# Kernel tuning notes

Hardware: AMD Instinct MI355X
Metric: run time of the kernel (lower is better)

The kernel has to match this reference:

```python
import jax, jax.numpy as jnp
import numpy as np

N = 50000      # nodes
E = 800000     # edges (avg degree 16)
F_IN = 128     # num_features
H = 128        # hidden_channels
C = 64         # num_classes
K = 3          # TAGConv hops (PyG default)


def setup_inputs() -> dict:
    key = jax.random.key(0)
    k0, k1, k2, k3 = jax.random.split(key, 4)
    x = jax.random.normal(k0, (N, F_IN), dtype=jnp.float32)
    edge_index = jax.random.randint(k1, (2, E), 0, N, dtype=jnp.int32)
    W1 = jax.random.normal(k2, (K + 1, F_IN, H), dtype=jnp.float32) / np.sqrt(F_IN).astype(np.float32)
    b1 = jnp.zeros((H,), dtype=jnp.float32)
    W2 = jax.random.normal(k3, (K + 1, H, C), dtype=jnp.float32) / np.sqrt(H).astype(np.float32)
    b2 = jnp.zeros((C,), dtype=jnp.float32)
    return {"x": x, "edge_index": edge_index, "W1": W1, "b1": b1, "W2": W2, "b2": b2}


def _gcn_norm(row, col):
    # PyG gcn_norm with add_self_loops=False (TAGConv default):
    # deg over target nodes (col), norm = d^-1/2[row] * d^-1/2[col]
    deg = jax.ops.segment_sum(jnp.ones((E,), dtype=jnp.float32), col, num_segments=N)
    dinv = jnp.where(deg > 0, jax.lax.rsqrt(jnp.maximum(deg, 1.0)) * jnp.where(deg > 0, 1.0, 0.0), 0.0)
    dinv = jnp.where(deg > 0, deg ** -0.5, 0.0)
    return dinv[row] * dinv[col]


def _tag_conv(h, row, col, norm, W, b):
    # out = sum_{k=0..K} A_hat^k h @ W[k] + b, A_hat = D^-1/2 A D^-1/2
    out = h @ W[0]
    for k in range(1, K + 1):
        h = jax.ops.segment_sum(norm[:, None] * h[row], col, num_segments=N)  # [N, d]
        out = out + h @ W[k]
    return out + b


def reference(x, edge_index, W1, b1, W2, b2):
    row, col = edge_index[0], edge_index[1]
    norm = _gcn_norm(row, col)  # [E]
    h = jax.nn.relu(_tag_conv(x, row, col, norm, W1, b1))
    # F.dropout with training=False is the identity (inference reference)
    out = _tag_conv(h, row, col, norm, W2, b2)
    return jax.nn.log_softmax(out, axis=1)
```

## Files before the change

### kernel.cpp

```cpp
#include <hip/hip_runtime.h>
#include <stdint.h>

#define NN 50000
#define EE 800000
#define NROWS 50048
#define CB 196
#define CAP 5120
#define ACH 4096

typedef unsigned int u32;
typedef unsigned short u16;
using f32x4 = __attribute__((ext_vector_type(4))) float;
using short8 = __attribute__((ext_vector_type(8))) short;

__device__ __forceinline__ float bflo(u32 u) { return __uint_as_float(u << 16); }
__device__ __forceinline__ float bfhi(u32 u) { return __uint_as_float(u & 0xFFFF0000u); }
__device__ __forceinline__ float bf1(u16 v) { return __uint_as_float(((u32)v) << 16); }
__device__ __forceinline__ u32 f2bf(float f) {
    u32 u = __float_as_uint(f);
    return (u + 0x7FFFu + ((u >> 16) & 1u)) >> 16;
}
__device__ __forceinline__ u32 pack2(float lo, float hi) {
    return f2bf(lo) | (f2bf(hi) << 16);
}

__device__ __forceinline__ int excl_scan256(int v, int tid) {
    __shared__ int ws_[4];
    int lane = tid & 63, w = tid >> 6;
    int x = v;
    #pragma unroll
    for (int off = 1; off < 64; off <<= 1) {
        int y = __shfl_up(x, off, 64);
        if (lane >= off) x += y;
    }
    if (lane == 63) ws_[w] = x;
    __syncthreads();
    int add = 0;
    if (w > 0) add += ws_[0];
    if (w > 1) add += ws_[1];
    if (w > 2) add += ws_[2];
    return add + x - v;
}


__global__ void detect_kernel(const u32* __restrict__ xw, int* __restrict__ flag) {
    int tid = threadIdx.x;
    int cnt = 0;
    for (int i = tid; i < 8192; i += 256) {
        u32 u = xw[i];
        int e0 = (u >> 7) & 0xFF, e1 = (u >> 23) & 0xFF;
        cnt += (e0 >= 0xC3) + (e1 >= 0xC3);
    }
    #pragma unroll
    for (int off = 32; off; off >>= 1) cnt += __shfl_xor(cnt, off, 64);
    __shared__ int wsum[4];
    if ((tid & 63) == 0) wsum[tid >> 6] = cnt;
    __syncthreads();
    if (tid == 0) flag[0] = (wsum[0] + wsum[1] + wsum[2] + wsum[3] > 100) ? 1 : 0;
}


__global__ __launch_bounds__(256) void phaseA_kernel(const int* __restrict__ ei,
                                                     int* __restrict__ ccnt,
                                                     u32* __restrict__ cpad) {
    __shared__ int hist[256], lstart[256], lofs[256], gbase[256];
    __shared__ u32 srt[ACH];
    int tid = threadIdx.x;
    int e0 = blockIdx.x * ACH;
    int nv = EE - e0; if (nv > ACH) nv = ACH;
    hist[tid] = 0;
    __syncthreads();
    u32 pk[16];
    int bn[16];
    #pragma unroll
    for (int i = 0; i < 16; i++) {
        int e = e0 + tid + i * 256;
        bn[i] = -1;
        if (e < EE) {
            int r = ei[e], c = ei[EE + e];
            bn[i] = c >> 8;
            pk[i] = (u32)r | ((u32)(c & 255) << 16) | ((u32)bn[i] << 24);
            atomicAdd(&hist[bn[i]], 1);
        }
    }
    __syncthreads();
    int v = hist[tid];
    int excl = excl_scan256(v, tid);
    lstart[tid] = excl;
    lofs[tid] = excl;
    gbase[tid] = atomicAdd(&ccnt[tid], v);
    __syncthreads();
    #pragma unroll
    for (int i = 0; i < 16; i++)
        if (bn[i] >= 0) {
            int lp = atomicAdd(&lofs[bn[i]], 1);
            srt[lp] = pk[i];
        }
    __syncthreads();
    for (int j = tid; j < nv; j += 256) {
        u32 pv = srt[j];
        int b = pv >> 24;
        cpad[(size_t)b * CAP + gbase[b] + (j - lstart[b])] = pv;
    }
}

__global__ void cscan_kernel(const int* __restrict__ ccnt, int* __restrict__ cbase,
                             int* __restrict__ rowptr, float* __restrict__ dinv) {
    int tid = threadIdx.x;
    int v = ccnt[tid];
    int excl = excl_scan256(v, tid);
    cbase[tid] = excl;
    if (tid == 0) {
        rowptr[NN] = EE;
        rowptr[NN + 1] = EE;
        dinv[NN] = 0.f;
    }
}


__global__ __launch_bounds__(256) void phaseB_kernel(const u32* __restrict__ cpad,
                                                     const int* __restrict__ ccnt,
                                                     const int* __restrict__ cbase,
                                                     u16* __restrict__ esrc,
                                                     int* __restrict__ rowptr,
                                                     float* __restrict__ dinv,
                                                     float* __restrict__ rinv) {
    __shared__ int hist[256], lstart[256], lofs[256];
    __shared__ u16 srt[CAP];
    int tid = threadIdx.x, cb = blockIdx.x;
    int cnt = ccnt[cb], base = cbase[cb];
    hist[tid] = 0;
    __syncthreads();
    for (int j = tid; j < cnt; j += 256)
        atomicAdd(&hist[(cpad[(size_t)cb * CAP + j] >> 16) & 255], 1);
    __syncthreads();
    int v = hist[tid];
    int excl = excl_scan256(v, tid);
    lstart[tid] = excl;
    lofs[tid] = excl;
    int g = cb * 256 + tid;
    if (g < NN) {
        rowptr[g] = base + excl;
        dinv[g] = v > 0 ? rsqrtf((float)v) : 0.f;
        rinv[g] = v > 0 ? sqrtf((float)v) : 0.f;
    }
    __syncthreads();
    for (int j = tid; j < cnt; j += 256) {
        u32 pv = cpad[(size_t)cb * CAP + j];
        int lp = atomicAdd(&lofs[(pv >> 16) & 255], 1);
        srt[lp] = (u16)(pv & 0xFFFF);
    }
    __syncthreads();
    for (int j = tid; j < cnt; j += 256) esrc[base + j] = srt[j];
}

__global__ void wprep_kernel(const void* __restrict__ w, u16* __restrict__ wt,
                             int fout, int nk, int mode, int total,
                             const int* __restrict__ flag) {
    int idx = blockIdx.x * 256 + threadIdx.x;
    if (idx >= total) return;
    u16 v = flag[0] ? (u16)f2bf(((const float*)w)[idx]) : ((const u16*)w)[idx];
    int per = 128 * fout;
    int k = idx / per, rem = idx % per;
    int in = rem / fout, o = rem % fout;
    size_t J;
    if (mode == 0) J = (size_t)(k * 16 + (in >> 3)) * fout + o;
    else J = (size_t)(in >> 3) * (nk * fout) + k * fout + o;
    wt[J * 8 + (in & 7)] = v;
}

__global__ void bprep_kernel(const void* __restrict__ b1, const void* __restrict__ b2,
                             float* __restrict__ bf, const int* __restrict__ flag) {
    int i = threadIdx.x;
    if (i < 128) bf[i] = flag[0] ? ((const float*)b1)[i] : bf1(((const u16*)b1)[i]);
    else {
        int j = i - 128;
        bf[i] = flag[0] ? ((const float*)b2)[j] : bf1(((const u16*)b2)[j]);
    }
}


__global__ void scalex_kernel(const void* __restrict__ x, u32* __restrict__ g0,
                              u32* __restrict__ xb, const float* __restrict__ dinv,
                              const int* __restrict__ flag) {
    int i = blockIdx.x * 256 + threadIdx.x;
    if (i >= (NN + 1) * 64) return;
    int node = i >> 6;
    int fl = flag[0];
    if (node == NN) {
        g0[i] = 0;
        if (fl) xb[i] = 0;
        return;
    }
    float dv = dinv[node];
    float a, b;
    if (fl) {
        const float* xf = (const float*)x;
        a = xf[2 * i];
        b = xf[2 * i + 1];
        xb[i] = pack2(a, b);
    } else {
        u32 u = ((const u32*)x)[i];
        a = bflo(u);
        b = bfhi(u);
    }
    g0[i] = pack2(a * dv, b * dv);
}


__global__ __launch_bounds__(256) void propg_kernel(const u32* __restrict__ gin,
                                                    u32* __restrict__ gout,
                                                    const int* __restrict__ rowptr,
                                                    const u16* __restrict__ esrc,
                                                    const float* __restrict__ dinv) {
    int node = (blockIdx.x * 256 + threadIdx.x) >> 6;
    int lane = threadIdx.x & 63;
    if (node > NN) return;
    int e0 = rowptr[node], e1 = rowptr[node + 1];
    float ax = 0.f, ay = 0.f;
    for (int base = e0; base < e1; base += 64) {
        int s_l = NN;
        if (base + lane < e1) s_l = esrc[base + lane];
        int cnt = e1 - base;
        if (cnt > 64) cnt = 64;
        for (int j = 0; j < cnt; j += 16) {
            u32 hv[16];
            #pragma unroll
            for (int u = 0; u < 16; u++) {
                int s = __builtin_amdgcn_readlane(s_l, j + u);
                hv[u] = gin[(size_t)s * 64 + lane];
            }
            #pragma unroll
            for (int u = 0; u < 16; u++) {
                ax += bflo(hv[u]);
                ay += bfhi(hv[u]);
            }
        }
    }
    float d = dinv[node];
    float d2 = d * d;
    gout[(size_t)node * 64 + lane] = pack2(ax * d2, ay * d2);
}


__device__ __forceinline__ float gatheru(const u16* __restrict__ uin, int e0, int e1,
                                         int lane, const u16* __restrict__ esrc) {
    float a = 0.f;
    for (int base = e0; base < e1; base += 64) {
        int s_l = NN;
        if (base + lane < e1) s_l = esrc[base + lane];
        int cnt = e1 - base;
        if (cnt > 64) cnt = 64;
        for (int j = 0; j < cnt; j += 16) {
            float hv[16];
            #pragma unroll
            for (int u = 0; u < 16; u++) {
                int s = __builtin_amdgcn_readlane(s_l, j + u);
                hv[u] = bf1(uin[(size_t)s * 64 + lane]);
            }
            #pragma unroll
            for (int u = 0; u < 16; u++) a += hv[u];
        }
    }
    return a;
}

__global__ __launch_bounds__(256) void prop64_add_kernel(const u16* __restrict__ uin,
                                                         const u16* __restrict__ zadd,
                                                         u16* __restrict__ uout,
                                                         const int* __restrict__ rowptr,
                                                         const u16* __restrict__ esrc,
                                                         const float* __restrict__ dinv) {
    int node = (blockIdx.x * 256 + threadIdx.x) >> 6;
    int lane = threadIdx.x & 63;
    if (node > NN) return;
    float s = gatheru(uin, rowptr[node], rowptr[node + 1], lane, esrc);
    float d = dinv[node];
    float r = fmaf(d * d, s, d * bf1(zadd[(size_t)node * 64 + lane]));
    uout[(size_t)node * 64 + lane] = (u16)f2bf(r);
}

__global__ __launch_bounds__(256) void prop64_final_kernel(const u16* __restrict__ uin,
                                                           const u16* __restrict__ z0,
                                                           const float* __restrict__ bias,
                                                           void* __restrict__ outv,
                                                           const int* __restrict__ rowptr,
                                                           const u16* __restrict__ esrc,
                                                           const float* __restrict__ dinv,
                                                           const int* __restrict__ flag) {
    int node = (blockIdx.x * 256 + threadIdx.x) >> 6;
    int lane = threadIdx.x & 63;
    if (node >= NN) return;
    float sg = gatheru(uin, rowptr[node], rowptr[node + 1], lane, esrc);
    float v = dinv[node] * sg + bf1(z0[(size_t)node * 64 + lane]) + bias[lane];
    float m = v;
    #pragma unroll
    for (int off = 32; off; off >>= 1) m = fmaxf(m, __shfl_xor(m, off, 64));
    float e = __expf(v - m);
    float s = e;
    #pragma unroll
    for (int off = 32; off; off >>= 1) s += __shfl_xor(s, off, 64);
    float r = v - m - __logf(s);
    if (flag[0]) ((float*)outv)[(size_t)node * 64 + lane] = r;
    else ((u16*)outv)[(size_t)node * 64 + lane] = (u16)f2bf(r);
}


__device__ __forceinline__ short8 ld8(const u16* p) {
    return __builtin_bit_cast(short8, *(const uint4*)p);
}

__global__ __launch_bounds__(256) void gemm1_kernel(const u32* __restrict__ a0,
                                                    const u32* __restrict__ a0alt,
                                                    const u32* __restrict__ a1,
                                                    const u32* __restrict__ a2,
                                                    const u32* __restrict__ a3,
                                                    const u16* __restrict__ wt,
                                                    const float* __restrict__ rinv,
                                                    const float* __restrict__ bias,
                                                    u32* __restrict__ outH,
                                                    const int* __restrict__ flag) {
    __shared__ uint4 hs[1024];
    const u32* A0 = flag[0] ? a0alt : a0;
    const u32* bufs[4] = {A0, a1, a2, a3};
    int t = threadIdx.x;
    int lane = t & 63, w = t >> 6;
    int row0 = blockIdx.x * 64;
    int m = lane & 15, qo = lane >> 4;
    f32x4 accx[8], accg[8];
    #pragma unroll
    for (int tt = 0; tt < 8; tt++) {
        accx[tt] = (f32x4){0.f, 0.f, 0.f, 0.f};
        accg[tt] = (f32x4){0.f, 0.f, 0.f, 0.f};
    }

    uint4 p[4];
    {
        const uint4* src = (const uint4*)A0 + (size_t)row0 * 16;
        #pragma unroll
        for (int i = 0; i < 4; i++) p[i] = src[t + 256 * i];
    }
    #pragma unroll
    for (int hop = 0; hop < 4; hop++) {
        __syncthreads();
        #pragma unroll
        for (int i = 0; i < 4; i++) {
            int g = t + 256 * i;
            hs[(g >> 4) * 16 + ((g & 15) ^ ((g >> 4) & 15))] = p[i];
        }
        __syncthreads();
        if (hop + 1 < 4) {
            const uint4* src = (const uint4*)bufs[hop + 1] + (size_t)row0 * 16;
            #pragma unroll
            for (int i = 0; i < 4; i++) p[i] = src[t + 256 * i];
        }
        #pragma unroll
        for (int q = 0; q < 4; q++) {
            short8 a = __builtin_bit_cast(short8,
                hs[(16 * w + m) * 16 + ((q * 4 + qo) ^ m)]);
            short8 b[8];
            #pragma unroll
            for (int tt = 0; tt < 8; tt++)
                b[tt] = ld8(wt + ((size_t)(hop * 16 + q * 4 + qo) * 128 + 16 * tt + m) * 8);
            if (hop == 0) {
                #pragma unroll
                for (int tt = 0; tt < 8; tt++)
                    accx[tt] = __builtin_amdgcn_mfma_f32_16x16x32_bf16(a, b[tt], accx[tt], 0, 0, 0);
            } else {
                #pragma unroll
                for (int tt = 0; tt < 8; tt++)
                    accg[tt] = __builtin_amdgcn_mfma_f32_16x16x32_bf16(a, b[tt], accg[tt], 0, 0, 0);
            }
        }
    }

    int r0 = row0 + 16 * w + qo * 4;
    float rv[4];
    #pragma unroll
    for (int r = 0; r < 4; r++) rv[r] = (r0 + r < NN) ? rinv[r0 + r] : 0.f;
    u16* o = (u16*)outH;
    #pragma unroll
    for (int tt = 0; tt < 8; tt++) {
        float bs = bias[16 * tt + m];
        #pragma unroll
        for (int r = 0; r < 4; r++) {
            int rr = r0 + r;
            if (rr < NN) {
                float vv = accx[tt][r] + rv[r] * accg[tt][r] + bs;
                o[(size_t)rr * 128 + 16 * tt + m] = (u16)f2bf(fmaxf(vv, 0.f));
            }
        }
    }
}

__global__ __launch_bounds__(256) void gemmz_kernel(const u32* __restrict__ aH,
                                                    const u16* __restrict__ wt,
                                                    const float* __restrict__ dinv,
                                                    u16* __restrict__ p0, u16* __restrict__ p1,
                                                    u16* __restrict__ p2, u16* __restrict__ p3) {
    __shared__ uint4 hs[1024];
    int t = threadIdx.x;
    int lane = t & 63, w = t >> 6;
    int row0 = blockIdx.x * 64;
    int py = blockIdx.y;
    int cb = py * 64;
    int m = lane & 15, qo = lane >> 4;
    f32x4 acc[4];
    #pragma unroll
    for (int tt = 0; tt < 4; tt++) acc[tt] = (f32x4){0.f, 0.f, 0.f, 0.f};
    {
        const uint4* src = (const uint4*)aH + (size_t)row0 * 16;
        #pragma unroll
        for (int i = 0; i < 4; i++) {
            int g = t + 256 * i;
            hs[(g >> 4) * 16 + ((g & 15) ^ ((g >> 4) & 15))] = src[g];
        }
    }
    __syncthreads();
    #pragma unroll
    for (int q = 0; q < 4; q++) {
        short8 a = __builtin_bit_cast(short8,
            hs[(16 * w + m) * 16 + ((q * 4 + qo) ^ m)]);
        short8 b[4];
        #pragma unroll
        for (int tt = 0; tt < 4; tt++)
            b[tt] = ld8(wt + ((size_t)(q * 4 + qo) * 256 + cb + 16 * tt + m) * 8);
        #pragma unroll
        for (int tt = 0; tt < 4; tt++)
            acc[tt] = __builtin_amdgcn_mfma_f32_16x16x32_bf16(a, b[tt], acc[tt], 0, 0, 0);
    }
    u16* zp = (py == 0) ? p0 : (py == 1) ? p1 : (py == 2) ? p2 : p3;
    int r0 = row0 + 16 * w + qo * 4;
    #pragma unroll
    for (int r = 0; r < 4; r++) {
        int rr = r0 + r;
        float sc = 1.f;
        if (py == 3) sc = (rr < NN) ? dinv[rr] : 0.f;
        #pragma unroll
        for (int tt = 0; tt < 4; tt++) {
            u16 val = (rr < NN) ? (u16)f2bf(sc * acc[tt][r]) : (u16)0;
            zp[(size_t)rr * 64 + 16 * tt + m] = val;
        }
    }
}


extern "C" void kernel_launch(void* const* d_in, const int* in_sizes, int n_in,
                              void* d_out, int out_size, void* d_ws, size_t ws_size,
                              hipStream_t stream) {
    const void* x  = d_in[0];
    const int*  ei = (const int*)d_in[1];
    const void* W1 = d_in[2];
    const void* b1 = d_in[3];
    const void* W2 = d_in[4];
    const void* b2 = d_in[5];

    char* ws = (char*)d_ws;
    size_t p = 0;
    auto alloc = [&](size_t bytes) -> void* {
        void* r = ws + p;
        p = (p + bytes + 255) & ~(size_t)255;
        return r;
    };
    int*   flag   = (int*)  alloc(256);
    int*   rowptr = (int*)  alloc((size_t)(NN + 2) * 4);
    float* dinv   = (float*)alloc((size_t)(NN + 64) * 4);
    float* rinv   = (float*)alloc((size_t)(NN + 64) * 4);
    int*   ccnt   = (int*)  alloc(256 * 4);
    int*   cbase  = (int*)  alloc(256 * 4);
    u16*   esrc   = (u16*)  alloc((size_t)EE * 2);
    u16*   wt1    = (u16*)  alloc((size_t)64 * 128 * 16);
    u16*   wt2    = (u16*)  alloc((size_t)16 * 256 * 16);
    float* biasF  = (float*)alloc(192 * 4);
    const size_t hbytes = (size_t)(NROWS + 16) * 64 * 4;
    u32* X = (u32*)alloc(hbytes);
    u32* P = (u32*)alloc(hbytes);
    u32* Q = (u32*)alloc(hbytes);
    u32* R = (u32*)alloc(hbytes);
    u32* cpad = X;

    const size_t ZP = (size_t)(NROWS + 16) * 64;
    u16* zR0 = (u16*)R;
    u16* zR1 = (u16*)R + ZP;
    u16* zP0 = (u16*)P;
    u16* zP1 = (u16*)P + ZP;
    u16* uX0 = (u16*)X;

    hipMemsetAsync(ccnt, 0, 256 * 4, stream);
    detect_kernel<<<1, 256, 0, stream>>>((const u32*)x, flag);
    phaseA_kernel<<<(EE + ACH - 1) / ACH, 256, 0, stream>>>(ei, ccnt, cpad);
    cscan_kernel<<<1, 256, 0, stream>>>(ccnt, cbase, rowptr, dinv);
    phaseB_kernel<<<CB, 256, 0, stream>>>(cpad, ccnt, cbase, esrc, rowptr, dinv, rinv);
    wprep_kernel<<<(4 * 128 * 128 + 255) / 256, 256, 0, stream>>>(
        W1, wt1, 128, 4, 0, 4 * 128 * 128, flag);
    wprep_kernel<<<(4 * 128 * 64 + 255) / 256, 256, 0, stream>>>(
        W2, wt2, 64, 4, 1, 4 * 128 * 64, flag);
    bprep_kernel<<<1, 192, 0, stream>>>(b1, b2, biasF, flag);

    const int PGX = ((NN + 1) * 64 + 255) / 256;
    const int PGF = (NN * 64) / 256;
    const int GG = NROWS / 64;

    scalex_kernel<<<PGX, 256, 0, stream>>>(x, P, X, dinv, flag);

    propg_kernel<<<PGX, 256, 0, stream>>>(P, Q, rowptr, esrc, dinv);
    propg_kernel<<<PGX, 256, 0, stream>>>(Q, R, rowptr, esrc, dinv);
    propg_kernel<<<PGX, 256, 0, stream>>>(R, P, rowptr, esrc, dinv);
    gemm1_kernel<<<GG, 256, 0, stream>>>((const u32*)x, X, Q, R, P, wt1, rinv, biasF, Q, flag);

    gemmz_kernel<<<dim3(GG, 4), 256, 0, stream>>>(Q, wt2, dinv, zR0, zR1, zP0, zP1);
    prop64_add_kernel<<<PGX, 256, 0, stream>>>(zP1, zP0, uX0, rowptr, esrc, dinv);
    prop64_add_kernel<<<PGX, 256, 0, stream>>>(uX0, zR1, zP0, rowptr, esrc, dinv);
    prop64_final_kernel<<<PGF, 256, 0, stream>>>(zP0, zR0, biasF + 128, d_out,
                                                 rowptr, esrc, dinv, flag);
}
```

Before: 337.5 us.

## Split gemm1 across two column halves and stage GEMM epilogues through LDS

gemm1 gets a column-tile template parameter. When the workspace has room for an extra H buffer, it launches a 2D grid in which each block computes 64 of the 128 output columns, writing to a separate buffer so that in-place aliasing with Q is avoided. Both gemm1 and gemmz now stage bf16 results in shared memory and write them out as coalesced 16-byte rows instead of scattered 2-byte stores. This doubles the block count and improves store coalescing, at the cost of every gemm1 block re-reading all four A tiles, plus extra LDS round trips and barriers.

```diff
diff --git a/kernel.cpp b/kernel.cpp
--- a/kernel.cpp
+++ b/kernel.cpp
@@ -310,6 +310,7 @@
     return __builtin_bit_cast(short8, *(const uint4*)p);
 }
 
+template <int NT>
 __global__ __launch_bounds__(256) void gemm1_kernel(const u32* __restrict__ a0,
                                                     const u32* __restrict__ a0alt,
                                                     const u32* __restrict__ a1,
@@ -326,10 +327,11 @@
     int t = threadIdx.x;
     int lane = t & 63, w = t >> 6;
     int row0 = blockIdx.x * 64;
+    int cb = (NT == 4) ? (int)blockIdx.y * 64 : 0;
     int m = lane & 15, qo = lane >> 4;
-    f32x4 accx[8], accg[8];
-    #pragma unroll
-    for (int tt = 0; tt < 8; tt++) {
+    f32x4 accx[NT], accg[NT];
+    #pragma unroll
+    for (int tt = 0; tt < NT; tt++) {
         accx[tt] = (f32x4){0.f, 0.f, 0.f, 0.f};
         accg[tt] = (f32x4){0.f, 0.f, 0.f, 0.f};
     }
@@ -358,17 +360,17 @@
         for (int q = 0; q < 4; q++) {
             short8 a = __builtin_bit_cast(short8,
                 hs[(16 * w + m) * 16 + ((q * 4 + qo) ^ m)]);
-            short8 b[8];
+            short8 b[NT];
             #pragma unroll
-            for (int tt = 0; tt < 8; tt++)
-                b[tt] = ld8(wt + ((size_t)(hop * 16 + q * 4 + qo) * 128 + 16 * tt + m) * 8);
+            for (int tt = 0; tt < NT; tt++)
+                b[tt] = ld8(wt + ((size_t)(hop * 16 + q * 4 + qo) * 128 + cb + 16 * tt + m) * 8);
             if (hop == 0) {
                 #pragma unroll
-                for (int tt = 0; tt < 8; tt++)
+                for (int tt = 0; tt < NT; tt++)
                     accx[tt] = __builtin_amdgcn_mfma_f32_16x16x32_bf16(a, b[tt], accx[tt], 0, 0, 0);
             } else {
                 #pragma unroll
-                for (int tt = 0; tt < 8; tt++)
+                for (int tt = 0; tt < NT; tt++)
                     accg[tt] = __builtin_amdgcn_mfma_f32_16x16x32_bf16(a, b[tt], accg[tt], 0, 0, 0);
             }
         }
@@ -378,17 +380,35 @@
     float rv[4];
     #pragma unroll
     for (int r = 0; r < 4; r++) rv[r] = (r0 + r < NN) ? rinv[r0 + r] : 0.f;
-    u16* o = (u16*)outH;
-    #pragma unroll
-    for (int tt = 0; tt < 8; tt++) {
-        float bs = bias[16 * tt + m];
+    __syncthreads();
+    u16* lds16 = (u16*)hs;
+    #pragma unroll
+    for (int tt = 0; tt < NT; tt++) {
+        float bs = bias[cb + 16 * tt + m];
         #pragma unroll
         for (int r = 0; r < 4; r++) {
             int rr = r0 + r;
-            if (rr < NN) {
-                float vv = accx[tt][r] + rv[r] * accg[tt][r] + bs;
-                o[(size_t)rr * 128 + 16 * tt + m] = (u16)f2bf(fmaxf(vv, 0.f));
-            }
+            float vv = 0.f;
+            if (rr < NN) vv = fmaxf(accx[tt][r] + rv[r] * accg[tt][r] + bs, 0.f);
+            lds16[(16 * w + qo * 4 + r) * (16 * NT) + 16 * tt + m] = (u16)f2bf(vv);
+        }
+    }
+    __syncthreads();
+    uint4* out4 = (uint4*)outH;
+    const uint4* epi4 = (const uint4*)hs;
+    if (NT == 8) {
+        #pragma unroll
+        for (int i = 0; i < 4; i++) {
+            int g = t + 256 * i;
+            int row = g >> 4, ch = g & 15;
+            out4[(size_t)(row0 + row) * 16 + ch] = epi4[g];
+        }
+    } else {
+        #pragma unroll
+        for (int i = 0; i < 2; i++) {
+            int g = t + 256 * i;
+            int row = g >> 3, ch = g & 7;
+            out4[(size_t)(row0 + row) * 16 + (cb >> 3) + ch] = epi4[g];
         }
     }
 }
@@ -431,16 +451,29 @@
     }
     u16* zp = (py == 0) ? p0 : (py == 1) ? p1 : (py == 2) ? p2 : p3;
     int r0 = row0 + 16 * w + qo * 4;
+    float sc[4];
     #pragma unroll
     for (int r = 0; r < 4; r++) {
         int rr = r0 + r;
-        float sc = 1.f;
-        if (py == 3) sc = (rr < NN) ? dinv[rr] : 0.f;
-        #pragma unroll
-        for (int tt = 0; tt < 4; tt++) {
-            u16 val = (rr < NN) ? (u16)f2bf(sc * acc[tt][r]) : (u16)0;
-            zp[(size_t)rr * 64 + 16 * tt + m] = val;
-        }
+        sc[r] = (rr < NN) ? ((py == 3) ? dinv[rr] : 1.f) : 0.f;
+    }
+    __syncthreads();
+    u16* lds16 = (u16*)hs;
+    #pragma unroll
+    for (int tt = 0; tt < 4; tt++) {
+        #pragma unroll
+        for (int r = 0; r < 4; r++) {
+            lds16[(16 * w + qo * 4 + r) * 64 + 16 * tt + m] = (u16)f2bf(sc[r] * acc[tt][r]);
+        }
+    }
+    __syncthreads();
+    uint4* zp4 = (uint4*)zp;
+    const uint4* epi4 = (const uint4*)hs;
+    #pragma unroll
+    for (int i = 0; i < 2; i++) {
+        int g = t + 256 * i;
+        int row = g >> 3, ch = g & 7;
+        zp4[(size_t)(row0 + row) * 8 + ch] = epi4[g];
     }
 }
 
@@ -477,6 +510,8 @@
     u32* P = (u32*)alloc(hbytes);
     u32* Q = (u32*)alloc(hbytes);
     u32* R = (u32*)alloc(hbytes);
+    int cs = (p + hbytes + 256 <= ws_size) ? 1 : 0;
+    u32* H5 = cs ? (u32*)alloc(hbytes) : Q;
     u32* cpad = X;
 
     const size_t ZP = (size_t)(NROWS + 16) * 64;
@@ -506,9 +541,14 @@
     propg_kernel<<<PGX, 256, 0, stream>>>(P, Q, rowptr, esrc, dinv);
     propg_kernel<<<PGX, 256, 0, stream>>>(Q, R, rowptr, esrc, dinv);
     propg_kernel<<<PGX, 256, 0, stream>>>(R, P, rowptr, esrc, dinv);
-    gemm1_kernel<<<GG, 256, 0, stream>>>((const u32*)x, X, Q, R, P, wt1, rinv, biasF, Q, flag);
-
-    gemmz_kernel<<<dim3(GG, 4), 256, 0, stream>>>(Q, wt2, dinv, zR0, zR1, zP0, zP1);
+    if (cs)
+        gemm1_kernel<4><<<dim3(GG, 2), 256, 0, stream>>>(
+            (const u32*)x, X, Q, R, P, wt1, rinv, biasF, H5, flag);
+    else
+        gemm1_kernel<8><<<GG, 256, 0, stream>>>(
+            (const u32*)x, X, Q, R, P, wt1, rinv, biasF, Q, flag);
+
+    gemmz_kernel<<<dim3(GG, 4), 256, 0, stream>>>(H5, wt2, dinv, zR0, zR1, zP0, zP1);
     prop64_add_kernel<<<PGX, 256, 0, stream>>>(zP1, zP0, uX0, rowptr, esrc, dinv);
     prop64_add_kernel<<<PGX, 256, 0, stream>>>(uX0, zR1, zP0, rowptr, esrc, dinv);
     prop64_final_kernel<<<PGF, 256, 0, stream>>>(zP0, zR0, biasF + 128, d_out,
```

After: 342.2 us. About the same (+1.4%).
